# Kernel tuning notes

Hardware: AMD Instinct MI355X
Metric: run time of the kernel (lower is better)

Reference implementation:

```python
import jax, jax.numpy as jnp
import numpy as np

LSTM_DIM = 512
SENT_LEN = 384  # n words -> n+2 LSTM positions (START/STOP)


def _lstm_scan(xs, Wih, Whh, b):
    """Unidirectional LSTM over xs [T, D] -> hidden states [T, H]. torch gate order i,f,g,o."""
    H = Whh.shape[1]
    gx = xs @ Wih.T + b  # [T, 4H] precompute input contribution

    def step(carry, g_x):
        h, c = carry
        g = g_x + h @ Whh.T
        i, f, gg, o = jnp.split(g, 4)
        i = jax.nn.sigmoid(i); f = jax.nn.sigmoid(f); o = jax.nn.sigmoid(o)
        c = f * c + i * jnp.tanh(gg)
        h = o * jnp.tanh(c)
        return (h, c), h

    init = (jnp.zeros((H,), xs.dtype), jnp.zeros((H,), xs.dtype))
    _, hs = jax.lax.scan(step, init, gx)
    return hs  # [T, H]


def setup_inputs() -> dict:
    key = jax.random.key(0)
    ks = jax.random.split(key, 16)
    T = SENT_LEN + 2
    H = LSTM_DIM
    s = lambda fan: 1.0 / np.sqrt(fan)
    return {
        "tag_ids": jax.random.randint(ks[0], (T,), 0, 50, dtype=jnp.int32),
        "word_ids": jax.random.randint(ks[1], (T,), 0, 10000, dtype=jnp.int32),
        "tag_emb": jax.random.normal(ks[2], (50, 128), jnp.float32) * 0.1,
        "word_emb": jax.random.normal(ks[3], (10000, 384), jnp.float32) * 0.1,
        "Wf_ih": jax.random.normal(ks[4], (4 * H, 512), jnp.float32) * s(512),
        "Wf_hh": jax.random.normal(ks[5], (4 * H, H), jnp.float32) * s(H),
        "bf": jnp.zeros((4 * H,), jnp.float32),
        "Wb_ih": jax.random.normal(ks[6], (4 * H, 512), jnp.float32) * s(512),
        "Wb_hh": jax.random.normal(ks[7], (4 * H, H), jnp.float32) * s(H),
        "bb": jnp.zeros((4 * H,), jnp.float32),
        "W1": jax.random.normal(ks[8], (2 * H, 1024), jnp.float32) * s(2 * H),
        "b1": jnp.zeros((1024,), jnp.float32),
        "W2": jax.random.normal(ks[9], (1024, 128), jnp.float32) * s(1024),
        "b2": jnp.zeros((128,), jnp.float32),
        "V1": jax.random.normal(ks[10], (2 * H, 1024), jnp.float32) * s(2 * H),
        "c1": jnp.zeros((1024,), jnp.float32),
        "V2": jax.random.normal(ks[11], (1024, 1), jnp.float32) * s(1024),
        "c2": jnp.zeros((1,), jnp.float32),
    }


def reference(tag_ids, word_ids, tag_emb, word_emb,
              Wf_ih, Wf_hh, bf, Wb_ih, Wb_hh, bb,
              W1, b1, W2, b2, V1, c1, V2, c2):
    H = LSTM_DIM
    # Embedding lookup: concat tag+word embeddings per position  [T, 512]
    x = jnp.concatenate([tag_emb[tag_ids], word_emb[word_ids]], axis=-1)
    # Bidirectional LSTM: forward states and backward states, each [T, H]
    fwd = _lstm_scan(x, Wf_ih, Wf_hh, bf)
    bwd = _lstm_scan(x[::-1], Wb_ih, Wb_hh, bb)[::-1]
    n = x.shape[0] - 2  # sentence length
    # All spans (l, r), 0 <= l < r <= n  (batched superset of recursive decode)
    L, R = np.triu_indices(n + 1, k=1)  # static index arrays, S = n(n+1)/2
    # get_span_encoding: [fwd[r]-fwd[l] ; bwd[l+1]-bwd[r+1]]  -> [S, 2H]
    enc = jnp.concatenate([fwd[R] - fwd[L], bwd[L + 1] - bwd[R + 1]], axis=-1)
    # Feedforward forward(): x = W^T x + b per layer, ReLU between layers
    label_scores = jax.nn.relu(enc @ W1 + b1) @ W2 + b2   # [S, label_vocab]
    split_scores = jax.nn.relu(enc @ V1 + c1) @ V2 + c2   # [S, 1] per-span split scalar
    # split score of candidate s inside (l,r) = split_scores[(l,s)] + split_scores[(s,r)]
    return jnp.concatenate([label_scores, split_scores], axis=-1)  # [S, label_vocab+1]
```

## Files before the change

kernel.cpp:

```cpp
#include <hip/hip_runtime.h>

#define T_LEN 386
#define NSPAN 73920

typedef float v4f __attribute__((ext_vector_type(4)));

__device__ inline void llc_load8(const float* p, v4f& a, v4f& b) {
    asm volatile("global_load_dwordx4 %0, %2, off sc0 sc1\n\t"
                 "global_load_dwordx4 %1, %2, off offset:16 sc0 sc1\n\t"
                 "s_waitcnt vmcnt(0)"
                 : "=&v"(a), "=&v"(b) : "v"(p) : "memory");
}
__device__ inline void llc_store4(float* p, v4f v) {
    asm volatile("global_store_dwordx4 %0, %1, off sc0 sc1"
                 :: "v"(p), "v"(v) : "memory");
}

__device__ inline float fsigmoid(float x) { return 1.f / (1.f + __expf(-x)); }
__device__ inline float ftanh(float x) {
    x = fminf(fmaxf(x, -15.f), 15.f);
    float e = __expf(2.f * x);
    return (e - 1.f) / (e + 1.f);
}

__global__ void k_embed(const int* __restrict__ tag_ids, const int* __restrict__ word_ids,
                        const float* __restrict__ tag_emb, const float* __restrict__ word_emb,
                        float* __restrict__ x) {
    int t = blockIdx.x;
    int tid = threadIdx.x;
    int tr = tag_ids[t], wr = word_ids[t];
    x[t * 512 + tid] = tag_emb[tr * 128 + tid];
    for (int j = tid; j < 384; j += 128)
        x[t * 512 + 128 + j] = word_emb[wr * 384 + j];
}

__global__ void k_gx(const float* __restrict__ x,
                     const float* __restrict__ Wf, const float* __restrict__ bf,
                     const float* __restrict__ Wb, const float* __restrict__ bb,
                     float* __restrict__ gxf, float* __restrict__ gxb) {
    __shared__ float xs[32 * 512];
    int dir = blockIdx.z;
    const float* W = dir ? Wb : Wf;
    const float* bias = dir ? bb : bf;
    float* out = dir ? gxb : gxf;
    int nbase = blockIdx.x * 64;
    int tbase = blockIdx.y * 32;
    int tid = threadIdx.x;

    for (int i = tid; i < 32 * 128; i += 256) {
        int row = i >> 7, c4 = i & 127;
        int t = tbase + row;
        float4 v = make_float4(0.f, 0.f, 0.f, 0.f);
        if (t < T_LEN) {
            int src = dir ? (T_LEN - 1 - t) : t;
            v = ((const float4*)(x + src * 512))[c4];
        }
        ((float4*)xs)[i] = v;
    }
    __syncthreads();

    int col = tid >> 2;
    int kq = tid & 3;
    int n = nbase + col;
    const float4* wrow = (const float4*)(W + (long)n * 512);
    float acc[32];
#pragma unroll
    for (int r = 0; r < 32; ++r) acc[r] = 0.f;
#pragma unroll 2
    for (int it = 0; it < 32; ++it) {
        int k4 = it * 4 + kq;
        float4 w = wrow[k4];
#pragma unroll
        for (int r = 0; r < 32; ++r) {
            float4 xv = ((const float4*)(xs + r * 512))[k4];
            acc[r] += w.x * xv.x + w.y * xv.y + w.z * xv.z + w.w * xv.w;
        }
    }
#pragma unroll
    for (int r = 0; r < 32; ++r) {
        float v = acc[r];
        v += __shfl_xor(v, 1, 4);
        v += __shfl_xor(v, 2, 4);
        acc[r] = v;
    }
    if (kq == 0) {
        float bv = bias[n];
        for (int r = 0; r < 32; ++r) {
            int t = tbase + r;
            if (t < T_LEN) out[t * 2048 + n] = acc[r] + bv;
        }
    }
}

__global__ void k_poison(float* __restrict__ st) {
    int i = blockIdx.x * 256 + threadIdx.x;
    __hip_atomic_store(st + i, 2.0f, __ATOMIC_RELAXED, __HIP_MEMORY_SCOPE_AGENT);
}

__launch_bounds__(256, 1)
__global__ void k_scan(const float* __restrict__ gxf, const float* __restrict__ gxb,
                       const float* __restrict__ Wfhh, const float* __restrict__ Wbhh,
                       float* fwd, float* bwd) {
    __shared__ float gx_sh[T_LEN * 64];
    __shared__ float h_sh[2][512];
    int bid = blockIdx.x;
    int dir = bid >> 5;
    int w = bid & 31;
    int tid = threadIdx.x;
    const float* gx = dir ? gxb : gxf;
    const float* Whh = dir ? Wbhh : Wfhh;
    float* st = dir ? bwd : fwd;

    for (int idx = tid; idx < T_LEN * 64; idx += 256) {
        int t = idx >> 6, j = idx & 63;
        gx_sh[idx] = gx[t * 2048 + (j >> 4) * 512 + w * 16 + (j & 15)];
    }

    int u = tid >> 4;
    int r = tid & 15;
    int g = r >> 2;
    int kq = r & 3;
    int grow = g * 512 + w * 16 + u;
    float4 wreg[32];
    const float4* wsrc = (const float4*)(Whh + (long)grow * 512);
#pragma unroll
    for (int it = 0; it < 32; ++it) wreg[it] = wsrc[it * 4 + kq];
    float c = 0.f;
    int wave = tid >> 6;

    for (int ts = 0; ts < T_LEN; ++ts) {
        float* hbuf = h_sh[ts & 1];
        if (tid < 64) {
            if (ts == 0) {
                float4 z = make_float4(0.f, 0.f, 0.f, 0.f);
                *(float4*)(hbuf + tid * 8) = z;
                *(float4*)(hbuf + tid * 8 + 4) = z;
            } else {
                int srow = dir ? (T_LEN - ts) : (ts - 1);
                const float* src = st + srow * 512 + tid * 8;
                v4f a, b;
                for (;;) {
                    llc_load8(src, a, b);
                    bool bad = a.x == 2.f || a.y == 2.f || a.z == 2.f || a.w == 2.f ||
                               b.x == 2.f || b.y == 2.f || b.z == 2.f || b.w == 2.f;
                    if (!__any(bad)) break;
                }
                *(v4f*)(hbuf + tid * 8) = a;
                *(v4f*)(hbuf + tid * 8 + 4) = b;
            }
        }
        __syncthreads();

        const float4* hv = (const float4*)hbuf;
        float a0 = 0.f, a1 = 0.f, a2 = 0.f, a3 = 0.f;
#pragma unroll
        for (int it = 0; it < 32; ++it) {
            float4 h4 = hv[it * 4 + kq];
            float4 w4 = wreg[it];
            a0 += w4.x * h4.x; a1 += w4.y * h4.y;
            a2 += w4.z * h4.z; a3 += w4.w * h4.w;
        }
        float v = (a0 + a1) + (a2 + a3);
        v += __shfl_xor(v, 1, 4);
        v += __shfl_xor(v, 2, 4);
        float gi = __shfl(v, (u & 3) * 16 + 0, 64)  + gx_sh[ts * 64 + u];
        float gf = __shfl(v, (u & 3) * 16 + 4, 64)  + gx_sh[ts * 64 + 16 + u];
        float gg = __shfl(v, (u & 3) * 16 + 8, 64)  + gx_sh[ts * 64 + 32 + u];
        float go = __shfl(v, (u & 3) * 16 + 12, 64) + gx_sh[ts * 64 + 48 + u];
        float i_ = fsigmoid(gi);
        float f_ = fsigmoid(gf);
        float o_ = fsigmoid(go);
        c = f_ * c + i_ * ftanh(gg);
        float h = o_ * ftanh(c);
        float h0 = __shfl(h, 0, 64);
        float h1 = __shfl(h, 16, 64);
        float h2 = __shfl(h, 32, 64);
        float h3 = __shfl(h, 48, 64);
        if ((tid & 63) == 0) {
            int drow = dir ? (T_LEN - 1 - ts) : ts;
            v4f hv4;
            hv4.x = h0; hv4.y = h1; hv4.z = h2; hv4.w = h3;
            llc_store4(st + drow * 512 + w * 16 + wave * 4, hv4);
        }
    }
}

__global__ void k_tables(const float* __restrict__ fwd, const float* __restrict__ bwd,
                         const float* __restrict__ W1, const float* __restrict__ V1,
                         float* __restrict__ A, float* __restrict__ B,
                         float* __restrict__ AV, float* __restrict__ BV) {
    __shared__ float xs[32 * 512];
    int which = blockIdx.z;
    const float* S = (which & 1) ? bwd : fwd;
    const float* W = ((which >> 1) ? V1 : W1) + (which & 1) * 512 * 1024;
    float* out = which == 0 ? A : which == 1 ? B : which == 2 ? AV : BV;
    int nbase = blockIdx.x * 64, tbase = blockIdx.y * 32;
    int tid = threadIdx.x;

    for (int i = tid; i < 32 * 128; i += 256) {
        int row = i >> 7, c4 = i & 127;
        int t = tbase + row;
        float4 v = make_float4(0.f, 0.f, 0.f, 0.f);
        if (t < T_LEN) v = ((const float4*)(S + t * 512))[c4];
        ((float4*)xs)[i] = v;
    }
    __syncthreads();

    int cg = tid & 15;
    int rg = tid >> 4;
    int n = nbase + cg * 4;
    float4 acc0 = make_float4(0.f, 0.f, 0.f, 0.f);
    float4 acc1 = make_float4(0.f, 0.f, 0.f, 0.f);
#pragma unroll 4
    for (int k = 0; k < 512; ++k) {
        float4 wv = *(const float4*)(W + (long)k * 1024 + n);
        float x0 = xs[(rg * 2) * 512 + k];
        float x1 = xs[(rg * 2 + 1) * 512 + k];
        acc0.x += x0 * wv.x; acc0.y += x0 * wv.y; acc0.z += x0 * wv.z; acc0.w += x0 * wv.w;
        acc1.x += x1 * wv.x; acc1.y += x1 * wv.y; acc1.z += x1 * wv.z; acc1.w += x1 * wv.w;
    }
    int t0 = tbase + rg * 2, t1 = t0 + 1;
    if (t0 < T_LEN) *(float4*)(out + (long)t0 * 1024 + n) = acc0;
    if (t1 < T_LEN) *(float4*)(out + (long)t1 * 1024 + n) = acc1;
}

#define TS 64
#define KC 64
__launch_bounds__(256, 2)
__global__ void k_span(const float* __restrict__ A, const float* __restrict__ B,
                       const float* __restrict__ AV, const float* __restrict__ BV,
                       const float* __restrict__ W2, const float* __restrict__ b1,
                       const float* __restrict__ b2, const float* __restrict__ V2,
                       const float* __restrict__ c1, const float* __restrict__ c2,
                       float* __restrict__ out) {
    __shared__ float hid[TS][KC + 4];
    __shared__ float w2s[KC * 128];
    __shared__ int ls[TS], rs[TS];
    int tid = threadIdx.x;
    int wg = blockIdx.x;

    if (tid < TS) {
        int s = wg * TS + tid;
        float disc = 769.0f * 769.0f - 8.0f * (float)s;
        int l = (int)floorf((769.0f - sqrtf(disc)) * 0.5f);
        if (l < 0) l = 0;
        if (l > 383) l = 383;
#define OFF(L) ((L) * 384 - ((L) * ((L) - 1)) / 2)
        while (l + 1 <= 384 && OFF(l + 1) <= s) ++l;
        while (l > 0 && OFF(l) > s) --l;
        int r = l + 1 + (s - OFF(l));
        ls[tid] = l; rs[tid] = r;
    }
    float acc[8][4];
#pragma unroll
    for (int a = 0; a < 8; ++a)
#pragma unroll
        for (int b = 0; b < 4; ++b) acc[a][b] = 0.f;
    float vacc[4] = {0.f, 0.f, 0.f, 0.f};
    int chg = tid & 31, sgm = tid >> 5;
    int kq = tid & 15, sgb = tid >> 4;
    __syncthreads();

    for (int kb = 0; kb < 1024; kb += KC) {
        if (kb) __syncthreads();
        for (int i = tid; i < KC * 128 / 4; i += 256)
            ((float4*)w2s)[i] = ((const float4*)(W2 + kb * 128))[i];
        int ko = kb + kq * 4;
        float4 bv = *(const float4*)(b1 + ko);
        float4 cv = *(const float4*)(c1 + ko);
        float4 v2 = *(const float4*)(V2 + ko);
#pragma unroll
        for (int si = 0; si < 4; ++si) {
            int sp = sgb * 4 + si;
            int l = ls[sp], r = rs[sp];
            float4 ar = *(const float4*)(A + (long)r * 1024 + ko);
            float4 al = *(const float4*)(A + (long)l * 1024 + ko);
            float4 bl = *(const float4*)(B + (long)(l + 1) * 1024 + ko);
            float4 br = *(const float4*)(B + (long)(r + 1) * 1024 + ko);
            float4 hx;
            hx.x = fmaxf(ar.x - al.x + bl.x - br.x + bv.x, 0.f);
            hx.y = fmaxf(ar.y - al.y + bl.y - br.y + bv.y, 0.f);
            hx.z = fmaxf(ar.z - al.z + bl.z - br.z + bv.z, 0.f);
            hx.w = fmaxf(ar.w - al.w + bl.w - br.w + bv.w, 0.f);
            *(float4*)&hid[sp][kq * 4] = hx;
            float4 vr = *(const float4*)(AV + (long)r * 1024 + ko);
            float4 vl = *(const float4*)(AV + (long)l * 1024 + ko);
            float4 ul = *(const float4*)(BV + (long)(l + 1) * 1024 + ko);
            float4 ur = *(const float4*)(BV + (long)(r + 1) * 1024 + ko);
            float h0 = fmaxf(vr.x - vl.x + ul.x - ur.x + cv.x, 0.f);
            float h1 = fmaxf(vr.y - vl.y + ul.y - ur.y + cv.y, 0.f);
            float h2 = fmaxf(vr.z - vl.z + ul.z - ur.z + cv.z, 0.f);
            float h3 = fmaxf(vr.w - vl.w + ul.w - ur.w + cv.w, 0.f);
            vacc[si] += h0 * v2.x + h1 * v2.y + h2 * v2.z + h3 * v2.w;
        }
        __syncthreads();
#pragma unroll 2
        for (int k = 0; k < KC; k += 4) {
            float4 h4[8];
#pragma unroll
            for (int j2 = 0; j2 < 8; ++j2)
                h4[j2] = *(const float4*)&hid[sgm * 8 + j2][k];
#pragma unroll
            for (int kk = 0; kk < 4; ++kk) {
                float4 wv = *(const float4*)&w2s[(k + kk) * 128 + chg * 4];
#pragma unroll
                for (int j2 = 0; j2 < 8; ++j2) {
                    float hx = (&h4[j2].x)[kk];
                    acc[j2][0] += hx * wv.x; acc[j2][1] += hx * wv.y;
                    acc[j2][2] += hx * wv.z; acc[j2][3] += hx * wv.w;
                }
            }
        }
    }

    float4 b2v = *(const float4*)(b2 + chg * 4);
#pragma unroll
    for (int j2 = 0; j2 < 8; ++j2) {
        int s = wg * TS + sgm * 8 + j2;
        float* o = out + (long)s * 129 + chg * 4;
        o[0] = acc[j2][0] + b2v.x; o[1] = acc[j2][1] + b2v.y;
        o[2] = acc[j2][2] + b2v.z; o[3] = acc[j2][3] + b2v.w;
    }
    float c2v = c2[0];
#pragma unroll
    for (int si = 0; si < 4; ++si) {
        float v = vacc[si];
        for (int o = 8; o; o >>= 1) v += __shfl_xor(v, o, 16);
        if (kq == 0) out[(long)(wg * TS + sgb * 4 + si) * 129 + 128] = v + c2v;
    }
}

extern "C" void kernel_launch(void* const* d_in, const int* in_sizes, int n_in,
                              void* d_out, int out_size, void* d_ws, size_t ws_size,
                              hipStream_t stream) {
    const int* tag_ids  = (const int*)d_in[0];
    const int* word_ids = (const int*)d_in[1];
    const float* tag_emb  = (const float*)d_in[2];
    const float* word_emb = (const float*)d_in[3];
    const float* Wf_ih = (const float*)d_in[4];
    const float* Wf_hh = (const float*)d_in[5];
    const float* bf    = (const float*)d_in[6];
    const float* Wb_ih = (const float*)d_in[7];
    const float* Wb_hh = (const float*)d_in[8];
    const float* bb    = (const float*)d_in[9];
    const float* W1 = (const float*)d_in[10];
    const float* b1 = (const float*)d_in[11];
    const float* W2 = (const float*)d_in[12];
    const float* b2 = (const float*)d_in[13];
    const float* V1 = (const float*)d_in[14];
    const float* c1 = (const float*)d_in[15];
    const float* V2 = (const float*)d_in[16];
    const float* c2 = (const float*)d_in[17];

    float* ws = (float*)d_ws;
    float* x   = ws + 256;
    float* gxf = x + T_LEN * 512;
    float* gxb = gxf + T_LEN * 2048;
    float* fwd = gxb + T_LEN * 2048;
    float* bwd = fwd + T_LEN * 512;
    float* A   = bwd + T_LEN * 512;
    float* B   = A + T_LEN * 1024;
    float* AV  = B + T_LEN * 1024;
    float* BV  = AV + T_LEN * 1024;

    k_poison<<<(2 * T_LEN * 512) / 256, 256, 0, stream>>>(fwd);
    k_embed<<<T_LEN, 128, 0, stream>>>(tag_ids, word_ids, tag_emb, word_emb, x);
    k_gx<<<dim3(32, 13, 2), 256, 0, stream>>>(x, Wf_ih, bf, Wb_ih, bb, gxf, gxb);
    k_scan<<<64, 256, 0, stream>>>(gxf, gxb, Wf_hh, Wb_hh, fwd, bwd);
    k_tables<<<dim3(16, 13, 4), 256, 0, stream>>>(fwd, bwd, W1, V1, A, B, AV, BV);
    k_span<<<NSPAN / 64, 256, 0, stream>>>(A, B, AV, BV, W2, b1, b2, V2, c1, c2,
                                           (float*)d_out);
}
```

Baseline: 1.386 ms.

## Place LSTM scan blocks on one XCD and exchange hidden state via L2

Launches 256 scan blocks cooperatively and keeps only those with blockIdx%8 in {0,1}, so that under round-robin XCD dispatch each direction's 32 blocks share one XCD. The per-step hidden-state exchange then uses L2-scope (sc0) loads and stores instead of system-coherent sc0 sc1 accesses, to cut cross-block latency. A mirrored copy is also written with LLC-coherent stores, and readers fall back to it after 16 failed polls. This relies on an undocumented block-to-XCD mapping and adds an extra store per step, more poison work, and 192 idle blocks.

```diff
diff --git a/kernel.cpp b/kernel.cpp
--- a/kernel.cpp
+++ b/kernel.cpp
@@ -5,6 +5,16 @@
 
 typedef float v4f __attribute__((ext_vector_type(4)));
 
+__device__ inline void l2_load8(const float* p, v4f& a, v4f& b) {
+    asm volatile("global_load_dwordx4 %0, %2, off sc0\n\t"
+                 "global_load_dwordx4 %1, %2, off offset:16 sc0\n\t"
+                 "s_waitcnt vmcnt(0)"
+                 : "=&v"(a), "=&v"(b) : "v"(p) : "memory");
+}
+__device__ inline void l2_store4(float* p, v4f v) {
+    asm volatile("global_store_dwordx4 %0, %1, off sc0"
+                 :: "v"(p), "v"(v) : "memory");
+}
 __device__ inline void llc_load8(const float* p, v4f& a, v4f& b) {
     asm volatile("global_load_dwordx4 %0, %2, off sc0 sc1\n\t"
                  "global_load_dwordx4 %1, %2, off offset:16 sc0 sc1\n\t"
@@ -100,16 +110,18 @@
 __launch_bounds__(256, 1)
 __global__ void k_scan(const float* __restrict__ gxf, const float* __restrict__ gxb,
                        const float* __restrict__ Wfhh, const float* __restrict__ Wbhh,
-                       float* fwd, float* bwd) {
+                       float* fwd, float* bwd, float* fwdm, float* bwdm) {
     __shared__ float gx_sh[T_LEN * 64];
     __shared__ float h_sh[2][512];
     int bid = blockIdx.x;
-    int dir = bid >> 5;
-    int w = bid & 31;
+    int dir = bid & 7;
+    if (dir > 1) return;
+    int w = bid >> 3;
     int tid = threadIdx.x;
     const float* gx = dir ? gxb : gxf;
     const float* Whh = dir ? Wbhh : Wfhh;
-    float* st = dir ? bwd : fwd;
+    float* st  = dir ? bwd  : fwd;
+    float* stm = dir ? bwdm : fwdm;
 
     for (int idx = tid; idx < T_LEN * 64; idx += 256) {
         int t = idx >> 6, j = idx & 63;
@@ -137,13 +149,21 @@
                 *(float4*)(hbuf + tid * 8 + 4) = z;
             } else {
                 int srow = dir ? (T_LEN - ts) : (ts - 1);
-                const float* src = st + srow * 512 + tid * 8;
+                const float* src  = st  + srow * 512 + tid * 8;
+                const float* srcm = stm + srow * 512 + tid * 8;
                 v4f a, b;
+                int tries = 0;
                 for (;;) {
-                    llc_load8(src, a, b);
+                    l2_load8(src, a, b);
                     bool bad = a.x == 2.f || a.y == 2.f || a.z == 2.f || a.w == 2.f ||
                                b.x == 2.f || b.y == 2.f || b.z == 2.f || b.w == 2.f;
                     if (!__any(bad)) break;
+                    if (++tries > 16) {
+                        llc_load8(srcm, a, b);
+                        bad = a.x == 2.f || a.y == 2.f || a.z == 2.f || a.w == 2.f ||
+                              b.x == 2.f || b.y == 2.f || b.z == 2.f || b.w == 2.f;
+                        if (!__any(bad)) break;
+                    }
                 }
                 *(v4f*)(hbuf + tid * 8) = a;
                 *(v4f*)(hbuf + tid * 8 + 4) = b;
@@ -180,7 +200,8 @@
             int drow = dir ? (T_LEN - 1 - ts) : ts;
             v4f hv4;
             hv4.x = h0; hv4.y = h1; hv4.z = h2; hv4.w = h3;
-            llc_store4(st + drow * 512 + w * 16 + wave * 4, hv4);
+            l2_store4(st + drow * 512 + w * 16 + wave * 4, hv4);
+            llc_store4(stm + drow * 512 + w * 16 + wave * 4, hv4);
         }
     }
 }
@@ -353,20 +374,33 @@
     const float* c2 = (const float*)d_in[17];
 
     float* ws = (float*)d_ws;
-    float* x   = ws + 256;
-    float* gxf = x + T_LEN * 512;
-    float* gxb = gxf + T_LEN * 2048;
-    float* fwd = gxb + T_LEN * 2048;
-    float* bwd = fwd + T_LEN * 512;
-    float* A   = bwd + T_LEN * 512;
-    float* B   = A + T_LEN * 1024;
-    float* AV  = B + T_LEN * 1024;
-    float* BV  = AV + T_LEN * 1024;
-
-    k_poison<<<(2 * T_LEN * 512) / 256, 256, 0, stream>>>(fwd);
+    float* x    = ws + 256;
+    float* gxf  = x + T_LEN * 512;
+    float* gxb  = gxf + T_LEN * 2048;
+    float* fwd  = gxb + T_LEN * 2048;
+    float* bwd  = fwd + T_LEN * 512;
+    float* fwdm = bwd + T_LEN * 512;
+    float* bwdm = fwdm + T_LEN * 512;
+    float* A    = bwdm + T_LEN * 512;
+    float* B    = A + T_LEN * 1024;
+    float* AV   = B + T_LEN * 1024;
+    float* BV   = AV + T_LEN * 1024;
+
+    k_poison<<<(4 * T_LEN * 512) / 256, 256, 0, stream>>>(fwd);
     k_embed<<<T_LEN, 128, 0, stream>>>(tag_ids, word_ids, tag_emb, word_emb, x);
     k_gx<<<dim3(32, 13, 2), 256, 0, stream>>>(x, Wf_ih, bf, Wb_ih, bb, gxf, gxb);
-    k_scan<<<64, 256, 0, stream>>>(gxf, gxb, Wf_hh, Wb_hh, fwd, bwd);
+
+    {
+        void* args[] = {(void*)&gxf, (void*)&gxb, (void*)&Wf_hh, (void*)&Wb_hh,
+                        (void*)&fwd, (void*)&bwd, (void*)&fwdm, (void*)&bwdm};
+        hipError_t e = hipLaunchCooperativeKernel((const void*)k_scan, dim3(256),
+                                                  dim3(256), args, 0, stream);
+        if (e != hipSuccess) {
+            k_scan<<<256, 256, 0, stream>>>(gxf, gxb, Wf_hh, Wb_hh, fwd, bwd,
+                                            fwdm, bwdm);
+        }
+    }
+
     k_tables<<<dim3(16, 13, 4), 256, 0, stream>>>(fwd, bwd, W1, V1, A, B, AV, BV);
     k_span<<<NSPAN / 64, 256, 0, stream>>>(A, B, AV, BV, W2, b1, b2, V2, c1, c2,
                                            (float*)d_out);
```

Result: slower. 2.103 ms (+51.8%).
